# Kernel optimization log

Hardware: AMD Instinct MI355X
Metric: run time of the kernel (lower is better)

## Reference

```python
import jax, jax.numpy as jnp
import numpy as np

MARGIN = 0.2  # matches init_kwargs; margin > 0 -> relu hinge branch

N_PARTS, NUM_CLASSES, K_PER_CLASS, D_FEAT = 64, 32, 16, 256


def setup_inputs() -> dict:
    key = jax.random.key(0)
    m = NUM_CLASSES * K_PER_CLASS  # 512
    feature = jax.random.normal(key, (N_PARTS, m, D_FEAT), dtype=jnp.float32)
    # Structured P x K labels: masked_select(...).view(n, m, -1, 1) in the
    # original requires exactly K positives per anchor, so labels must be
    # K samples per class (identical across the part dimension).
    label = jnp.tile(jnp.repeat(jnp.arange(NUM_CLASSES, dtype=jnp.int64), K_PER_CLASS)[None, :], (N_PARTS, 1))
    return {"feature": feature, "label": label, "num_pos": K_PER_CLASS}


def _batch_euc_dist(x):
    # x: [n, m, d] -> dist: [n, m, m]
    x2 = jnp.sum(x * x, axis=2)  # [n, m]
    d2 = x2[:, :, None] + x2[:, None, :] - 2.0 * jnp.einsum('nid,njd->nij', x, x)
    return jnp.sqrt(jax.nn.relu(d2))


def reference(feature, label, num_pos):
    n, m, d = feature.shape
    dist = _batch_euc_dist(feature)  # [n, m, m]
    same = label[:, :, None] == label[:, None, :]  # [n, m, m] bool
    # masked_select preserves flat (row-major) order, so per anchor the
    # selected positives/negatives appear in increasing index order ->
    # stable argsort on the mask reproduces it exactly.
    pos_idx = jnp.argsort(jnp.where(same, 0, 1), axis=-1)[..., :num_pos]        # [n, m, k]
    neg_idx = jnp.argsort(jnp.where(same, 1, 0), axis=-1)[..., :m - num_pos]    # [n, m, m-k]
    hp = jnp.take_along_axis(dist, pos_idx, axis=-1)[:, :, :, None]   # [n, m, k, 1]
    hn = jnp.take_along_axis(dist, neg_idx, axis=-1)[:, :, None, :]   # [n, m, 1, m-k]
    # margin > 0 -> relu hinge (heter/hard/part mining disabled by init flags)
    loss = jax.nn.relu(MARGIN + hp - hn).reshape(n, -1)               # [n, m*k*(m-k)]
    nonzero_num = jnp.sum(loss != 0, axis=1).astype(loss.dtype)       # [n]
    loss_mean = jnp.where(nonzero_num == 0, 0.0,
                          jnp.sum(loss, axis=1) / jnp.maximum(nonzero_num, 1.0))
    return loss_mean.mean(), nonzero_num.mean()
```

## Files before the change

kernel.cpp:

```cpp
#include <hip/hip_runtime.h>
#include <math.h>


#define MARGIN 0.2f
constexpr int NP = 64;
constexpr int M = 512;
constexpr int D = 256;
constexpr int SDS = 20;

typedef __attribute__((ext_vector_type(8))) short bf16x8;
typedef __attribute__((ext_vector_type(4))) float f32x4;
typedef __attribute__((address_space(1))) const unsigned int as1_uint;
typedef __attribute__((address_space(3))) unsigned int as3_uint;

__device__ __forceinline__ unsigned f2bf(float x) {
  unsigned b = __float_as_uint(x);
  return (b + 0x7FFFu + ((b >> 16) & 1u)) >> 16;
}
__device__ __forceinline__ uint4 pack8u(float4 v0, float4 v1) {
  uint4 p;
  p.x = f2bf(v0.x) | (f2bf(v0.y) << 16);
  p.y = f2bf(v0.z) | (f2bf(v0.w) << 16);
  p.z = f2bf(v1.x) | (f2bf(v1.y) << 16);
  p.w = f2bf(v1.z) | (f2bf(v1.w) << 16);
  return p;
}
__device__ __forceinline__ float sq8(float4 v0, float4 v1) {
  return v0.x * v0.x + v0.y * v0.y + v0.z * v0.z + v0.w * v0.w +
         v1.x * v1.x + v1.y * v1.y + v1.z * v1.z + v1.w * v1.w;
}

__global__ __launch_bounds__(256) void convert_kernel(
    const float* __restrict__ feat, unsigned short* __restrict__ fb,
    float* __restrict__ x2g) {
  const int t = threadIdx.x;
  const int R = blockIdx.x * 8 + (t >> 5);
  const int c = t & 31;
  const int r = R & 63;
  const float* src = feat + (size_t)R * D + c * 8;
  float4 v0 = ((const float4*)src)[0], v1 = ((const float4*)src)[1];
  *(uint4*)&fb[((size_t)R * 32 + (c ^ (r & 7))) * 8] = pack8u(v0, v1);
  float ss = sq8(v0, v1);
  ss += __shfl_xor(ss, 16, 32);
  ss += __shfl_xor(ss, 8, 32);
  ss += __shfl_xor(ss, 4, 32);
  ss += __shfl_xor(ss, 2, 32);
  ss += __shfl_xor(ss, 1, 32);
  if (c == 0) x2g[R] = ss;
}

__global__ __launch_bounds__(512, 2) void triplet_kernel(
    const unsigned short* __restrict__ fb, const float* __restrict__ x2g,
    float* __restrict__ psum, float* __restrict__ pcnt) {
  __shared__ unsigned short Bs[64 * 32 * 8];
  __shared__ float sortd[64 * SDS];
  __shared__ float sumt[64 * SDS];
  __shared__ float x2s[2][64];
  __shared__ float reds[8], redc[8];

  const int p = blockIdx.x;
  const int diag = blockIdx.y;
  const int i0 = diag * 64;
  const int t = threadIdx.x;
  const int w = t >> 6, L = t & 63;
  const int rw = w & 3;
  const int fh = w >> 2;
  const int tx = L & 15, quad = L >> 4;
  const int tx7 = tx & 7;
  const float* x2p = x2g + (size_t)p * M;

  auto dma_tile = [&](int j0) {
    const char* gsrc = (const char*)fb + ((size_t)p * M + j0) * 512;
    char* lbase = (char*)Bs + w * 1024;
#pragma unroll
    for (int i = 0; i < 4; i++)
      __builtin_amdgcn_global_load_lds((as1_uint*)(gsrc + i * 8192 + t * 16),
                                       (as3_uint*)(lbase + i * 8192), 16, 0, 0);
  };

  dma_tile(i0);
  if (t < 64) x2s[0][t] = x2p[i0 + t];

  const size_t Ra = (size_t)p * M + i0 + rw * 16 + tx;
  bf16x8 af[8];
#pragma unroll
  for (int kc = 0; kc < 2; kc++)
#pragma unroll
    for (int ks = 0; ks < 4; ks++) {
      const int ca = kc * 16 + ks * 4 + quad;
      af[kc * 4 + ks] = *(const bf16x8*)&fb[(Ra * 32 + (ca ^ tx7)) * 8];
    }
  float x2i[4];
#pragma unroll
  for (int r = 0; r < 4; r++) x2i[r] = x2p[i0 + rw * 16 + quad * 4 + r];

  f32x4 srt[4][4];
  float hsum = 0.f;
  int hcnt = 0;

  for (int ti = 0; ti < 8; ti++) {
    const int cur = ti & 1;
    const int j0 = ((diag + ti) & 7) * 64;
    __syncthreads();

    f32x4 acc[2];
    acc[0] = (f32x4){0.f, 0.f, 0.f, 0.f};
    acc[1] = (f32x4){0.f, 0.f, 0.f, 0.f};
#pragma unroll
    for (int kc = 0; kc < 2; kc++)
#pragma unroll
      for (int ks = 0; ks < 4; ks++) {
        const bf16x8 a = af[kc * 4 + ks];
        const int cb = kc * 16 + ks * 4 + quad;
#pragma unroll
        for (int ff = 0; ff < 2; ff++) {
          const int rowb = (fh * 2 + ff) * 16 + tx;
          bf16x8 b = *(bf16x8*)&Bs[(rowb * 32 + (cb ^ tx7)) * 8];
          acc[ff] =
              __builtin_amdgcn_mfma_f32_16x16x32_bf16(a, b, acc[ff], 0, 0, 0);
        }
      }

    __syncthreads();

    const bool havenext = ti < 7;
    const int nj0 = ((diag + ti + 1) & 7) * 64;
    if (ti != 0 && havenext) {
      dma_tile(nj0);
      if (t < 64) x2s[(ti + 1) & 1][t] = x2p[nj0 + t];
    }

    if (ti == 0) {
      if ((rw >> 1) == fh) {
        const int ff = rw & 1;
        const float xj = x2s[0][rw * 16 + tx];
#pragma unroll
        for (int r = 0; r < 4; r++) {
          float d2 = x2i[r] + xj - 2.f * acc[ff][r];
          sortd[(rw * 16 + quad * 4 + r) * SDS + tx] =
              MARGIN + sqrtf(fmaxf(d2, 0.f));
        }
      }
      __syncthreads();
      if (t < 64) {
        float v[16];
#pragma unroll
        for (int q4 = 0; q4 < 4; q4++) {
          f32x4 vv = *(f32x4*)&sortd[t * SDS + q4 * 4];
          v[q4 * 4 + 0] = vv.x; v[q4 * 4 + 1] = vv.y;
          v[q4 * 4 + 2] = vv.z; v[q4 * 4 + 3] = vv.w;
        }
#pragma unroll
        for (int k = 2; k <= 16; k <<= 1)
#pragma unroll
          for (int j = k >> 1; j > 0; j >>= 1)
#pragma unroll
            for (int i = 0; i < 16; i++) {
              const int l = i ^ j;
              if (l > i) {
                const bool asc = ((i & k) == 0);
                if (asc ? (v[i] > v[l]) : (v[i] < v[l])) {
                  float tmp = v[i]; v[i] = v[l]; v[l] = tmp;
                }
              }
            }
#pragma unroll
        for (int q4 = 0; q4 < 4; q4++)
          *(f32x4*)&sortd[t * SDS + q4 * 4] =
              (f32x4){v[q4 * 4], v[q4 * 4 + 1], v[q4 * 4 + 2], v[q4 * 4 + 3]};
        float run = 0.f;
        sumt[t * SDS + 0] = 0.f;
#pragma unroll
        for (int c = 1; c <= 16; c++) {
          run += v[16 - c];
          sumt[t * SDS + c] = run;
        }
      }
      __syncthreads();
#pragma unroll
      for (int r = 0; r < 4; r++)
#pragma unroll
        for (int q4 = 0; q4 < 4; q4++)
          srt[r][q4] = *(f32x4*)&sortd[(rw * 16 + quad * 4 + r) * SDS + q4 * 4];

      if (havenext) {
        dma_tile(nj0);
        if (t < 64) x2s[1][t] = x2p[nj0 + t];
      }
    }

#pragma unroll
    for (int ff = 0; ff < 2; ff++) {
      const int f = fh * 2 + ff;
      if (ti == 0 && f == rw) continue;
      const float xj = x2s[cur][f * 16 + tx];
#pragma unroll
      for (int r = 0; r < 4; r++) {
        const float dn = sqrtf(fmaxf(x2i[r] + xj - 2.f * acc[ff][r], 0.f));
        int c = 0;
#define CMP(sv) c += ((sv) > dn) ? 1 : 0;
        CMP(srt[r][0].x) CMP(srt[r][0].y) CMP(srt[r][0].z) CMP(srt[r][0].w)
        CMP(srt[r][1].x) CMP(srt[r][1].y) CMP(srt[r][1].z) CMP(srt[r][1].w)
        CMP(srt[r][2].x) CMP(srt[r][2].y) CMP(srt[r][2].z) CMP(srt[r][2].w)
        CMP(srt[r][3].x) CMP(srt[r][3].y) CMP(srt[r][3].z) CMP(srt[r][3].w)
#undef CMP
        hsum += sumt[(rw * 16 + quad * 4 + r) * SDS + c];
        hsum = fmaf(-(float)c, dn, hsum);
        hcnt += c;
      }
    }
  }

  float cf = (float)hcnt;
  for (int off = 32; off > 0; off >>= 1) {
    hsum += __shfl_down(hsum, off, 64);
    cf += __shfl_down(cf, off, 64);
  }
  if (L == 0) { reds[w] = hsum; redc[w] = cf; }
  __syncthreads();
  if (t == 0) {
    float bs = 0.f, bc = 0.f;
#pragma unroll
    for (int i = 0; i < 8; i++) { bs += reds[i]; bc += redc[i]; }
    psum[p * 8 + diag] = bs;
    pcnt[p * 8 + diag] = bc;
  }
}

__global__ __launch_bounds__(64) void finalize_kernel(
    const float* __restrict__ psum, const float* __restrict__ pcnt,
    float* __restrict__ out) {
  const int p = threadIdx.x;
  float s = 0.f, c = 0.f;
#pragma unroll
  for (int i = 0; i < 8; i++) {
    s += psum[p * 8 + i];
    c += pcnt[p * 8 + i];
  }
  float lm = (c == 0.f) ? 0.f : s / fmaxf(c, 1.f);
  float ctot = c;
  for (int off = 32; off > 0; off >>= 1) {
    lm += __shfl_down(lm, off, 64);
    ctot += __shfl_down(ctot, off, 64);
  }
  if (p == 0) {
    out[0] = lm / 64.f;
    out[1] = ctot / 64.f;
  }
}

extern "C" void kernel_launch(void* const* d_in, const int* in_sizes, int n_in,
                              void* d_out, int out_size, void* d_ws,
                              size_t ws_size, hipStream_t stream) {
  const float* feat = (const float*)d_in[0];
  float* ws = (float*)d_ws;
  float* psum = ws;
  float* pcnt = ws + 512;
  float* x2g = ws + 1024;
  unsigned short* fb = (unsigned short*)(ws + 1024 + 32768);
  float* out = (float*)d_out;

  convert_kernel<<<(NP * M) / 8, 256, 0, stream>>>(feat, fb, x2g);
  dim3 grid(NP, 8);
  triplet_kernel<<<grid, 512, 0, stream>>>(fb, x2g, psum, pcnt);
  finalize_kernel<<<1, 64, 0, stream>>>(psum, pcnt, out);
}
```

Before: 125.0 us.

## Split triplet work into 32-row blocks and read sorted positives from LDS

Each block now handles 32 anchor rows instead of 64, doubling the grid to 64x16 so more blocks run concurrently. Each wave computes one 16x16 output tile instead of two. The per-row sorted positive distances are re-read from shared memory inside the hinge loop instead of being held in registers, which lowers register pressure at the cost of extra LDS traffic. Each block still loads the full B tiles, so global-to-LDS traffic per anchor row doubles, and the leftover srt register loads are effectively dead code.

```diff
diff --git a/kernel.cpp b/kernel.cpp
--- a/kernel.cpp
+++ b/kernel.cpp
@@ -53,20 +53,22 @@
     const unsigned short* __restrict__ fb, const float* __restrict__ x2g,
     float* __restrict__ psum, float* __restrict__ pcnt) {
   __shared__ unsigned short Bs[64 * 32 * 8];
-  __shared__ float sortd[64 * SDS];
-  __shared__ float sumt[64 * SDS];
+  __shared__ float sortd[32 * SDS];
+  __shared__ float sumt[32 * SDS];
   __shared__ float x2s[2][64];
   __shared__ float reds[8], redc[8];
 
   const int p = blockIdx.x;
-  const int diag = blockIdx.y;
-  const int i0 = diag * 64;
+  const int q = blockIdx.y;
+  const int i0 = q * 32;
+  const int T0 = q >> 1;
   const int t = threadIdx.x;
   const int w = t >> 6, L = t & 63;
-  const int rw = w & 3;
-  const int fh = w >> 2;
+  const int rw = w & 1;
+  const int f = w >> 1;
   const int tx = L & 15, quad = L >> 4;
   const int tx7 = tx & 7;
+  const int f_pos = ((q & 1) << 1) + rw;
   const float* x2p = x2g + (size_t)p * M;
 
   auto dma_tile = [&](int j0) {
@@ -78,8 +80,8 @@
                                        (as3_uint*)(lbase + i * 8192), 16, 0, 0);
   };
 
-  dma_tile(i0);
-  if (t < 64) x2s[0][t] = x2p[i0 + t];
+  dma_tile(T0 * 64);
+  if (t < 64) x2s[0][t] = x2p[T0 * 64 + t];
 
   const size_t Ra = (size_t)p * M + i0 + rw * 16 + tx;
   bf16x8 af[8];
@@ -94,55 +96,48 @@
 #pragma unroll
   for (int r = 0; r < 4; r++) x2i[r] = x2p[i0 + rw * 16 + quad * 4 + r];
 
-  f32x4 srt[4][4];
+  f32x4 srt[4];
   float hsum = 0.f;
   int hcnt = 0;
 
   for (int ti = 0; ti < 8; ti++) {
     const int cur = ti & 1;
-    const int j0 = ((diag + ti) & 7) * 64;
     __syncthreads();
 
-    f32x4 acc[2];
-    acc[0] = (f32x4){0.f, 0.f, 0.f, 0.f};
-    acc[1] = (f32x4){0.f, 0.f, 0.f, 0.f};
+    f32x4 acc = (f32x4){0.f, 0.f, 0.f, 0.f};
 #pragma unroll
     for (int kc = 0; kc < 2; kc++)
 #pragma unroll
       for (int ks = 0; ks < 4; ks++) {
-        const bf16x8 a = af[kc * 4 + ks];
         const int cb = kc * 16 + ks * 4 + quad;
-#pragma unroll
-        for (int ff = 0; ff < 2; ff++) {
-          const int rowb = (fh * 2 + ff) * 16 + tx;
-          bf16x8 b = *(bf16x8*)&Bs[(rowb * 32 + (cb ^ tx7)) * 8];
-          acc[ff] =
-              __builtin_amdgcn_mfma_f32_16x16x32_bf16(a, b, acc[ff], 0, 0, 0);
-        }
+        const int rowb = f * 16 + tx;
+        bf16x8 b = *(bf16x8*)&Bs[(rowb * 32 + (cb ^ tx7)) * 8];
+        acc = __builtin_amdgcn_mfma_f32_16x16x32_bf16(af[kc * 4 + ks], b, acc,
+                                                      0, 0, 0);
       }
 
     __syncthreads();
 
     const bool havenext = ti < 7;
-    const int nj0 = ((diag + ti + 1) & 7) * 64;
+    const int nj0 = ((T0 + ti + 1) & 7) * 64;
     if (ti != 0 && havenext) {
       dma_tile(nj0);
       if (t < 64) x2s[(ti + 1) & 1][t] = x2p[nj0 + t];
     }
 
+    const float xj = x2s[cur][f * 16 + tx];
+
     if (ti == 0) {
-      if ((rw >> 1) == fh) {
-        const int ff = rw & 1;
-        const float xj = x2s[0][rw * 16 + tx];
+      if (f == f_pos) {
 #pragma unroll
         for (int r = 0; r < 4; r++) {
-          float d2 = x2i[r] + xj - 2.f * acc[ff][r];
+          float d2 = x2i[r] + xj - 2.f * acc[r];
           sortd[(rw * 16 + quad * 4 + r) * SDS + tx] =
               MARGIN + sqrtf(fmaxf(d2, 0.f));
         }
       }
       __syncthreads();
-      if (t < 64) {
+      if (t < 32) {
         float v[16];
 #pragma unroll
         for (int q4 = 0; q4 < 4; q4++) {
@@ -178,33 +173,38 @@
       }
       __syncthreads();
 #pragma unroll
-      for (int r = 0; r < 4; r++)
-#pragma unroll
-        for (int q4 = 0; q4 < 4; q4++)
-          srt[r][q4] = *(f32x4*)&sortd[(rw * 16 + quad * 4 + r) * SDS + q4 * 4];
-
+      for (int q4 = 0; q4 < 4; q4++)
+        srt[q4] = *(f32x4*)&sortd[(rw * 16 + quad * 4 + (q4 & 3)) * SDS];
       if (havenext) {
         dma_tile(nj0);
         if (t < 64) x2s[1][t] = x2p[nj0 + t];
       }
     }
 
-#pragma unroll
-    for (int ff = 0; ff < 2; ff++) {
-      const int f = fh * 2 + ff;
-      if (ti == 0 && f == rw) continue;
-      const float xj = x2s[cur][f * 16 + tx];
+    if (!(ti == 0 && f == f_pos)) {
 #pragma unroll
       for (int r = 0; r < 4; r++) {
-        const float dn = sqrtf(fmaxf(x2i[r] + xj - 2.f * acc[ff][r], 0.f));
+        const int row = rw * 16 + quad * 4 + r;
+        if (ti == 0) {
+          if (r == 0) {
+#pragma unroll
+            for (int q4 = 0; q4 < 4; q4++)
+              srt[q4] = *(f32x4*)&sortd[row * SDS];
+          }
+        }
+        const float dn = sqrtf(fmaxf(x2i[r] + xj - 2.f * acc[r], 0.f));
+        f32x4 s0 = *(f32x4*)&sortd[row * SDS + 0];
+        f32x4 s1 = *(f32x4*)&sortd[row * SDS + 4];
+        f32x4 s2 = *(f32x4*)&sortd[row * SDS + 8];
+        f32x4 s3 = *(f32x4*)&sortd[row * SDS + 12];
         int c = 0;
 #define CMP(sv) c += ((sv) > dn) ? 1 : 0;
-        CMP(srt[r][0].x) CMP(srt[r][0].y) CMP(srt[r][0].z) CMP(srt[r][0].w)
-        CMP(srt[r][1].x) CMP(srt[r][1].y) CMP(srt[r][1].z) CMP(srt[r][1].w)
-        CMP(srt[r][2].x) CMP(srt[r][2].y) CMP(srt[r][2].z) CMP(srt[r][2].w)
-        CMP(srt[r][3].x) CMP(srt[r][3].y) CMP(srt[r][3].z) CMP(srt[r][3].w)
+        CMP(s0.x) CMP(s0.y) CMP(s0.z) CMP(s0.w)
+        CMP(s1.x) CMP(s1.y) CMP(s1.z) CMP(s1.w)
+        CMP(s2.x) CMP(s2.y) CMP(s2.z) CMP(s2.w)
+        CMP(s3.x) CMP(s3.y) CMP(s3.z) CMP(s3.w)
 #undef CMP
-        hsum += sumt[(rw * 16 + quad * 4 + r) * SDS + c];
+        hsum += sumt[row * SDS + c];
         hsum = fmaf(-(float)c, dn, hsum);
         hcnt += c;
       }
@@ -222,8 +222,8 @@
     float bs = 0.f, bc = 0.f;
 #pragma unroll
     for (int i = 0; i < 8; i++) { bs += reds[i]; bc += redc[i]; }
-    psum[p * 8 + diag] = bs;
-    pcnt[p * 8 + diag] = bc;
+    psum[p * 16 + q] = bs;
+    pcnt[p * 16 + q] = bc;
   }
 }
 
@@ -233,9 +233,9 @@
   const int p = threadIdx.x;
   float s = 0.f, c = 0.f;
 #pragma unroll
-  for (int i = 0; i < 8; i++) {
-    s += psum[p * 8 + i];
-    c += pcnt[p * 8 + i];
+  for (int i = 0; i < 16; i++) {
+    s += psum[p * 16 + i];
+    c += pcnt[p * 16 + i];
   }
   float lm = (c == 0.f) ? 0.f : s / fmaxf(c, 1.f);
   float ctot = c;
@@ -255,13 +255,13 @@
   const float* feat = (const float*)d_in[0];
   float* ws = (float*)d_ws;
   float* psum = ws;
-  float* pcnt = ws + 512;
-  float* x2g = ws + 1024;
-  unsigned short* fb = (unsigned short*)(ws + 1024 + 32768);
+  float* pcnt = ws + 1024;
+  float* x2g = ws + 2048;
+  unsigned short* fb = (unsigned short*)(ws + 2048 + 32768);
   float* out = (float*)d_out;
 
   convert_kernel<<<(NP * M) / 8, 256, 0, stream>>>(feat, fb, x2g);
-  dim3 grid(NP, 8);
+  dim3 grid(NP, 16);
   triplet_kernel<<<grid, 512, 0, stream>>>(fb, x2g, psum, pcnt);
   finalize_kernel<<<1, 64, 0, stream>>>(psum, pcnt, out);
 }
```

Measured after the change: 121.0 us. 3.2% less time.
